# Kernel optimization log

Hardware: AMD Instinct MI355X
Metric: run time of the kernel (lower is better)

Reference implementation:

```python
import jax, jax.numpy as jnp
import numpy as np
from jax import lax

B, N, IN, OUT, RANK, P = 8, 7057, 1024, 1024, 64, 84
ALPHA = 1
SCALING = ALPHA / RANK
RATES = (2, 1, 4)


def _cubic(t):
    # PyTorch bicubic kernel (a = -0.75)
    a = -0.75
    at = jnp.abs(t)
    w1 = ((a + 2.0) * at - (a + 3.0)) * at * at + 1.0
    w2 = (((at - 5.0) * at + 8.0) * at - 4.0) * a
    return jnp.where(at <= 1.0, w1, jnp.where(at < 2.0, w2, 0.0))


def _resize_axis(x, out_size, axis):
    # 1-D bicubic resize along `axis`, align_corners=False, border replicate
    in_size = x.shape[axis]
    scale = in_size / out_size
    src = (jnp.arange(out_size, dtype=jnp.float32) + 0.5) * scale - 0.5
    i0 = jnp.floor(src)
    offs = jnp.arange(-1, 3, dtype=jnp.float32)[:, None]  # [4,1]
    pos = i0[None, :] + offs                              # [4,out]
    w = _cubic(src[None, :] - pos)                        # [4,out]
    idx = jnp.clip(pos.astype(jnp.int32), 0, in_size - 1)
    g = jnp.take(x, idx, axis=axis)  # axis -> (4, out)
    wshape = [1] * g.ndim
    wshape[axis] = 4
    wshape[axis + 1] = out_size
    return jnp.sum(g * w.reshape(wshape), axis=axis)


def _bicubic(x, h, w):
    # x: [B,C,H,W] -> [B,C,h,w]
    x = _resize_axis(x, h, axis=2)
    return _resize_axis(x, w, axis=3)


def _expert(x, cw, cb, rate):
    # x: [B,C,H,W]; cw: [C,C,3,3]; cb: [C]
    b, c, h, w = x.shape
    y = _bicubic(x, h * rate, w * rate)
    y = lax.conv_general_dilated(y, cw, (1, 1), [(1, 1), (1, 1)],
                                 dimension_numbers=('NCHW', 'OIHW', 'NCHW'))
    y = y + cb[None, :, None, None]
    y = _bicubic(y, h, w)
    return y.transpose(0, 2, 3, 1).reshape(b, h * w, c)  # [B,HW,C]


def setup_inputs() -> dict:
    key = jax.random.key(0)
    ks = jax.random.split(key, 9)
    return {
        'x': jax.random.normal(ks[0], (B, N, IN), dtype=jnp.float32),
        'W0': jax.random.normal(ks[1], (OUT, IN), dtype=jnp.float32) * 0.02,
        'b0': jax.random.normal(ks[2], (OUT,), dtype=jnp.float32) * 0.02,
        'W_down': jax.random.normal(ks[3], (RANK, IN), dtype=jnp.float32) * 0.02,
        'W_gate': jax.random.uniform(ks[4], (3, RANK), dtype=jnp.float32),
        'b_gate': jax.random.normal(ks[5], (3,), dtype=jnp.float32) * 0.02,
        'conv_w': jax.random.normal(ks[6], (3, RANK, RANK, 3, 3), dtype=jnp.float32) * 0.05,
        'conv_b': jax.random.normal(ks[7], (3, RANK), dtype=jnp.float32) * 0.02,
        'W_up': jax.random.normal(ks[8], (OUT, RANK), dtype=jnp.float32) * 0.02,
    }


def reference(x, W0, b0, W_down, W_gate, b_gate, conv_w, conv_b, W_up):
    out = jnp.einsum('bni,oi->bno', x, W0) + b0            # original layer
    z = jnp.einsum('bni,ri->bnr', x, W_down)               # lora_down (dropout p=0)
    cls_embed = z[:, :1]                                    # [B,1,R]
    feat = z[:, 1:].reshape(B, P, P, RANK).transpose(0, 3, 1, 2)  # [B,R,P,P]
    pooled = feat.mean(axis=(2, 3))                         # AdaptiveAvgPool2d(1)
    gate_score = pooled @ W_gate.T + b_gate                 # [B,3]
    gate_idx = jnp.argmax(gate_score, axis=-1)              # [B]
    eouts = jnp.stack([_expert(feat, conv_w[i], conv_b[i], RATES[i])
                       for i in range(3)], axis=0)          # [3,B,HW,R]
    sel = eouts[gate_idx, jnp.arange(B)] * SCALING          # [B,HW,R]
    lora = jnp.concatenate([cls_embed, sel], axis=1)        # [B,N,R]
    lora_out = jnp.einsum('bnr,or->bno', lora, W_up)
    return out + lora_out
```

## Files before the change

### kernel.cpp

```cpp
#include <hip/hip_runtime.h>
#include <stdint.h>

typedef unsigned short u16;
typedef __bf16 bf16x8 __attribute__((ext_vector_type(8)));
typedef float f32x4 __attribute__((ext_vector_type(4)));

#define B_ 8
#define N_ 7057
#define MTOT 56456
#define SCALING_F (1.0f/64.0f)

#define Z_OFF    0ull
#define LORA_OFF 14452736ull
#define GIDX_OFF 21679104ull
#define CWT_OFF  21679360ull
#define W0B_OFF  21900544ull
#define WDB_OFF  23997696ull
#define WUB_OFF  24128768ull
#define UP_OFF   24259840ull
#define CO_OFF   139865344ull
#define XB_OFF   255470848ull
#define WS_FAST  371092736ull
#define UPB_STRIDE ((size_t)112896 * 64)

__device__ __forceinline__ u16 f2b(float f) {
  __bf16 h = (__bf16)f;
  union { __bf16 h; u16 u; } v; v.h = h; return v.u;
}
__device__ __forceinline__ float b2f(u16 u) {
  union { uint32_t i; float f; } v; v.i = ((uint32_t)u) << 16; return v.f;
}
__device__ __forceinline__ void gload_lds16(const void* g, void* l) {
  __builtin_amdgcn_global_load_lds(
      (const __attribute__((address_space(1))) uint32_t*)g,
      (__attribute__((address_space(3))) uint32_t*)l, 16, 0, 0);
}
__device__ __forceinline__ f32x4 mfma16(bf16x8 a, bf16x8 b, f32x4 c) {
  return __builtin_amdgcn_mfma_f32_16x16x32_bf16(a, b, c, 0, 0, 0);
}
__device__ __forceinline__ bf16x8 cvt8(float4 a, float4 b) {
  bf16x8 v;
  v[0] = (__bf16)a.x; v[1] = (__bf16)a.y; v[2] = (__bf16)a.z; v[3] = (__bf16)a.w;
  v[4] = (__bf16)b.x; v[5] = (__bf16)b.y; v[6] = (__bf16)b.z; v[7] = (__bf16)b.w;
  return v;
}
__device__ __forceinline__ float cubicw(float t) {
  const float a = -0.75f;
  float at = fabsf(t);
  float w1 = ((a + 2.0f) * at - (a + 3.0f)) * at * at + 1.0f;
  float w2 = (((at - 5.0f) * at + 8.0f) * at - 4.0f) * a;
  return at <= 1.0f ? w1 : (at < 2.0f ? w2 : 0.0f);
}
__device__ __forceinline__ int iclamp(int v, int lo, int hi) { return v < lo ? lo : (v > hi ? hi : v); }
__device__ __forceinline__ int rate_of(int e) { return e == 0 ? 2 : (e == 1 ? 1 : 4); }

__global__ __launch_bounds__(256) void cvtall_kernel(const float* __restrict__ W0, const float* __restrict__ Wd,
                                                     const float* __restrict__ Wup, u16* __restrict__ dst) {
  int i = (blockIdx.x * 256 + threadIdx.x) * 4;
  if (i >= 1179648) return;
  const float* src;
  if (i < 1048576)      src = W0 + i;
  else if (i < 1114112) src = Wd + (i - 1048576);
  else                  src = Wup + (i - 1114112);
  float4 v = *(const float4*)src;
  union { u16 u[4]; uint2 q; } p;
  p.u[0] = f2b(v.x); p.u[1] = f2b(v.y); p.u[2] = f2b(v.z); p.u[3] = f2b(v.w);
  *(uint2*)(dst + i) = p.q;
}

__global__ __launch_bounds__(256) void cvtx_kernel(const float* __restrict__ x, u16* __restrict__ xb) {
  size_t stride = (size_t)gridDim.x * 256 * 8;
  for (size_t i = ((size_t)blockIdx.x * 256 + threadIdx.x) * 8; i < (size_t)MTOT * 1024; i += stride) {
    float4 a = *(const float4*)(x + i);
    float4 b = *(const float4*)(x + i + 4);
    *(bf16x8*)(xb + i) = cvt8(a, b);
  }
}

__global__ __launch_bounds__(256) void zgemm_kernel(const float* __restrict__ x,
                                                    const u16* __restrict__ Wdb,
                                                    float* __restrict__ z,
                                                    u16* __restrict__ xb) {
  __shared__ u16 As[64 * 32];
  __shared__ u16 Bs[64 * 32];
  const int tid = threadIdx.x;
  const int lane = tid & 63;
  const int w = tid >> 6;
  const int row0 = blockIdx.x * 64;
  f32x4 acc[4] = {{0,0,0,0},{0,0,0,0},{0,0,0,0},{0,0,0,0}};
  const int srow = tid >> 2, sk8 = tid & 3;
  int arow = row0 + srow; if (arow >= MTOT) arow = MTOT - 1;
  const float* agf = x + (size_t)arow * 1024 + sk8 * 8;
  const u16* bg = Wdb + (size_t)srow * 1024 + sk8 * 8;
  u16* xbp = xb ? (xb + (size_t)arow * 1024 + sk8 * 8) : nullptr;
  u16* al = As + tid * 8;
  u16* bl = Bs + tid * 8;
  const int klo = (lane >> 4) * 8;
  for (int k0 = 0; k0 < 1024; k0 += 32) {
    gload_lds16(bg + k0, bl);
    float4 q0 = *(const float4*)(agf + k0);
    float4 q1 = *(const float4*)(agf + k0 + 4);
    bf16x8 cv = cvt8(q0, q1);
    *(bf16x8*)al = cv;
    if (xbp) *(bf16x8*)(xbp + k0) = cv;
    __syncthreads();
    bf16x8 a = *(const bf16x8*)(As + (w * 16 + (lane & 15)) * 32 + klo);
#pragma unroll
    for (int fc = 0; fc < 4; ++fc) {
      bf16x8 bb = *(const bf16x8*)(Bs + (fc * 16 + (lane & 15)) * 32 + klo);
      acc[fc] = mfma16(a, bb, acc[fc]);
    }
    __syncthreads();
  }
  const int crow = (lane >> 4) * 4, ccol = lane & 15;
#pragma unroll
  for (int fc = 0; fc < 4; ++fc) {
#pragma unroll
    for (int i = 0; i < 4; ++i) {
      int gr = row0 + w * 16 + crow + i;
      if (gr < MTOT) z[(size_t)gr * 64 + fc * 16 + ccol] = acc[fc][i];
    }
  }
}

__global__ __launch_bounds__(256) void convwt_kernel(const float* __restrict__ cw, u16* __restrict__ cwt) {
  int idx = blockIdx.x * 256 + threadIdx.x;
  if (idx >= 3 * 9 * 64 * 64) return;
  int ci = idx & 63;
  int co = (idx >> 6) & 63;
  int rest = idx >> 12;
  int tap = rest % 9;
  int e = rest / 9;
  int sw = ((((ci >> 3) ^ (co & 7)) << 3) | (ci & 7));
  cwt[(((size_t)rest * 64) + co) * 64 + sw] = f2b(cw[((size_t)(e * 64 + co) * 64 + ci) * 9 + tap]);
}

__global__ __launch_bounds__(256) void gate1_kernel(const float* __restrict__ z, float* __restrict__ pp) {
  int b = blockIdx.y, q = blockIdx.x;
  int tid = threadIdx.x;
  int c = tid & 63, part = tid >> 6;
  const float* zb = z + (size_t)b * N_ * 64;
  int n0 = 1 + q * 126;
  float s = 0.0f;
  for (int n = n0 + part; n < n0 + 126; n += 4) s += zb[(size_t)n * 64 + c];
  __shared__ float red[4][64];
  red[part][c] = s;
  __syncthreads();
  if (tid < 64)
    pp[((size_t)b * 56 + q) * 64 + tid] = red[0][tid] + red[1][tid] + red[2][tid] + red[3][tid];
}

__global__ __launch_bounds__(64) void gate2_kernel(const float* __restrict__ pp, const float* __restrict__ z,
                                                   const float* __restrict__ Wg, const float* __restrict__ bg,
                                                   int* __restrict__ gidx, u16* __restrict__ lora) {
  int b = blockIdx.x;
  int c = threadIdx.x;
  float s = 0.0f;
  for (int q = 0; q < 56; ++q) s += pp[((size_t)b * 56 + q) * 64 + c];
  __shared__ float pl[64];
  pl[c] = s * (1.0f / 7056.0f);
  const float* zb = z + (size_t)b * N_ * 64;
  lora[(size_t)b * N_ * 64 + c] = f2b(zb[c]);
  __syncthreads();
  if (c == 0) {
    float best = 0.0f; int bi = 0;
    for (int e = 0; e < 3; ++e) {
      float sc = bg[e];
      for (int r = 0; r < 64; ++r) sc += pl[r] * Wg[e * 64 + r];
      if (e == 0 || sc > best) { best = sc; bi = e; }
    }
    gidx[b] = bi;
  }
}

__global__ __launch_bounds__(256) void conv_kernel(const float* __restrict__ z, const u16* __restrict__ cwt,
                                                   const float* __restrict__ cb, const int* __restrict__ gidx,
                                                   u16* __restrict__ cvo) {
  int b = blockIdx.z;
  int e = gidx[b];
  int r = rate_of(e);
  int H = 84 * r;
  int tx = blockIdx.x, ty = blockIdx.y;
  if (tx * 8 >= H || ty * 8 >= H) return;
  __shared__ u16 halo[100 * 64];
  __shared__ u16 Bw[2][4096];
  __shared__ float hw[100][8];
  __shared__ int hidx[100][8];
  int tid = threadIdx.x, lane = tid & 63, w = tid >> 6;
  const float* zb = z + ((size_t)b * N_ + 1) * 64;
  const u16* wte = cwt + (size_t)e * 9 * 4096;
  gload_lds16(wte + tid * 8, Bw[0] + tid * 8);
  gload_lds16(wte + 2048 + tid * 8, Bw[0] + 2048 + tid * 8);
  float inv = 1.0f / (float)r;
  if (tid < 100) {
    int hy = tid / 10, hx = tid - hy * 10;
    int iy = ty * 8 - 1 + hy, ix = tx * 8 - 1 + hx;
    float sy = (iy + 0.5f) * inv - 0.5f;
    float fy = floorf(sy);
    int iy0 = (int)fy;
    float sx = (ix + 0.5f) * inv - 0.5f;
    float fx = floorf(sx);
    int ix0 = (int)fx;
#pragma unroll
    for (int u = 0; u < 4; ++u) {
      hw[tid][u] = cubicw(sy - (fy - 1.0f + u));
      hidx[tid][u] = iclamp(iy0 - 1 + u, 0, 83) * (84 * 64);
      hw[tid][4 + u] = cubicw(sx - (fx - 1.0f + u));
      hidx[tid][4 + u] = iclamp(ix0 - 1 + u, 0, 83) * 64;
    }
  }
  __syncthreads();
  for (int li = tid; li < 800; li += 256) {
    int pix = li >> 3, cq = li & 7;
    int hy = pix / 10, hx = pix - hy * 10;
    int iy = ty * 8 - 1 + hy, ix = tx * 8 - 1 + hx;
    bf16x8 o;
#pragma unroll
    for (int t = 0; t < 8; ++t) o[t] = (__bf16)0.0f;
    if (iy >= 0 && iy < H && ix >= 0 && ix < H) {
      float a8[8] = {0.f,0.f,0.f,0.f,0.f,0.f,0.f,0.f};
#pragma unroll
      for (int u = 0; u < 4; ++u) {
        const float* zr = zb + hidx[pix][u] + cq * 8;
        float wyu = hw[pix][u];
#pragma unroll
        for (int v = 0; v < 4; ++v) {
          float wuv = wyu * hw[pix][4 + v];
          const float* zp = zr + hidx[pix][4 + v];
          float4 q0 = *(const float4*)zp;
          float4 q1 = *(const float4*)(zp + 4);
          a8[0] += wuv * q0.x; a8[1] += wuv * q0.y; a8[2] += wuv * q0.z; a8[3] += wuv * q0.w;
          a8[4] += wuv * q1.x; a8[5] += wuv * q1.y; a8[6] += wuv * q1.z; a8[7] += wuv * q1.w;
        }
      }
#pragma unroll
      for (int t = 0; t < 8; ++t) o[t] = (__bf16)a8[t];
    }
    *(bf16x8*)(halo + pix * 64 + (((cq ^ (pix & 7)) << 3))) = o;
  }
  __syncthreads();
  f32x4 acc[4] = {{0,0,0,0},{0,0,0,0},{0,0,0,0},{0,0,0,0}};
  int p = w * 16 + (lane & 15);
  int py = p >> 3, px = p & 7;
  int kg = lane >> 4;
  for (int tap = 0; tap < 9; ++tap) {
    if (tap < 8) {
      const u16* wt = wte + (size_t)(tap + 1) * 4096;
      gload_lds16(wt + tid * 8, Bw[(tap + 1) & 1] + tid * 8);
      gload_lds16(wt + 2048 + tid * 8, Bw[(tap + 1) & 1] + 2048 + tid * 8);
    }
    int dy = tap / 3, dx = tap - dy * 3;
    int pr = (py + dy) * 10 + (px + dx);
    const u16* bwc = Bw[tap & 1];
#pragma unroll
    for (int kk = 0; kk < 2; ++kk) {
      int ch = kk * 4 + kg;
      bf16x8 a = *(const bf16x8*)(halo + pr * 64 + (((ch ^ (pr & 7)) << 3)));
#pragma unroll
      for (int fc = 0; fc < 4; ++fc) {
        int co = fc * 16 + (lane & 15);
        bf16x8 bb = *(const bf16x8*)(bwc + co * 64 + (((ch ^ (co & 7)) << 3)));
        acc[fc] = mfma16(a, bb, acc[fc]);
      }
    }
    __syncthreads();
  }
  int crow = (lane >> 4) * 4, ccol = lane & 15;
  u16* cvb = cvo + (size_t)b * UPB_STRIDE;
#pragma unroll
  for (int fc = 0; fc < 4; ++fc) {
    int co = fc * 16 + ccol;
    float bias = cb[e * 64 + co];
#pragma unroll
    for (int i = 0; i < 4; ++i) {
      int pd = w * 16 + crow + i;
      int gy = ty * 8 + (pd >> 3), gx = tx * 8 + (pd & 7);
      if (gy < H && gx < H)
        cvb[((size_t)gy * H + gx) * 64 + co] = f2b(acc[fc][i] + bias);
    }
  }
}

__global__ __launch_bounds__(256) void down_kernel(const u16* __restrict__ cvo, const int* __restrict__ gidx,
                                                   u16* __restrict__ lora) {
  int b = blockIdx.z;
  int r = rate_of(gidx[b]);
  int H = 84 * r;
  int tid = threadIdx.x;
  int c = tid & 63, s = tid >> 6;
  int y = blockIdx.y;
  int x = blockIdx.x * 4 + s;
  float fr = (float)r;
  float sy = (y + 0.5f) * fr - 0.5f;
  float fy = floorf(sy);
  int iy0 = (int)fy;
  float wy[4]; int yi[4];
#pragma unroll
  for (int u = 0; u < 4; ++u) { wy[u] = cubicw(sy - (fy - 1.0f + u)); yi[u] = iclamp(iy0 - 1 + u, 0, H - 1); }
  float sx = (x + 0.5f) * fr - 0.5f;
  float fx = floorf(sx);
  int ix0 = (int)fx;
  float wx[4]; int xi[4];
#pragma unroll
  for (int v = 0; v < 4; ++v) { wx[v] = cubicw(sx - (fx - 1.0f + v)); xi[v] = iclamp(ix0 - 1 + v, 0, H - 1); }
  const u16* cbase = cvo + (size_t)b * UPB_STRIDE;
  float acc = 0.0f;
#pragma unroll
  for (int u = 0; u < 4; ++u)
#pragma unroll
    for (int v = 0; v < 4; ++v)
      acc += wy[u] * wx[v] * b2f(cbase[((size_t)yi[u] * H + xi[v]) * 64 + c]);
  lora[((size_t)b * N_ + 1 + y * 84 + x) * 64 + c] = f2b(acc * SCALING_F);
}

__global__ __launch_bounds__(256) void main_gemm(const u16* __restrict__ xb, const u16* __restrict__ W0b,
                                                 const float* __restrict__ b0, const u16* __restrict__ lora,
                                                 const u16* __restrict__ Wub, float* __restrict__ out) {
  __shared__ u16 As[128 * 64];
  __shared__ u16 Bs[128 * 64];
  int tid = threadIdx.x, lane = tid & 63, w = tid >> 6;
  int bid = blockIdx.x;
  int wg = (bid & 7) * 442 + (bid >> 3);
  int row0 = (wg >> 3) * 128, col0 = (wg & 7) * 128;
  int wr = w >> 1, wc = w & 1;
  f32x4 acc[4][4] = {};
  int srow = tid >> 3;
  int schunk = tid & 7;
  int sch8 = ((schunk ^ (srow & 7)) << 3);
  int ar[4]; int br[4];
  u16* aldst[4]; u16* bldst[4];
#pragma unroll
  for (int p = 0; p < 4; ++p) {
    int rr = row0 + p * 32 + srow;
    ar[p] = rr >= MTOT ? MTOT - 1 : rr;
    br[p] = col0 + p * 32 + srow;
    aldst[p] = As + (p * 32 + srow) * 64 + schunk * 8;
    bldst[p] = Bs + (p * 32 + srow) * 64 + schunk * 8;
  }
  for (int k0 = 0; k0 < 1024; k0 += 64) {
#pragma unroll
    for (int p = 0; p < 4; ++p)
      gload_lds16(xb + (size_t)ar[p] * 1024 + k0 + sch8, aldst[p]);
#pragma unroll
    for (int p = 0; p < 4; ++p)
      gload_lds16(W0b + (size_t)br[p] * 1024 + k0 + sch8, bldst[p]);
    __syncthreads();
#pragma unroll
    for (int kk = 0; kk < 2; ++kk) {
      int pc = (((kk << 2) + (lane >> 4)) ^ (lane & 7)) << 3;
      bf16x8 af[4], bfr[4];
#pragma unroll
      for (int fm = 0; fm < 4; ++fm)
        af[fm] = *(const bf16x8*)(As + (wr * 64 + fm * 16 + (lane & 15)) * 64 + pc);
#pragma unroll
      for (int fc = 0; fc < 4; ++fc)
        bfr[fc] = *(const bf16x8*)(Bs + (wc * 64 + fc * 16 + (lane & 15)) * 64 + pc);
#pragma unroll
      for (int fm = 0; fm < 4; ++fm)
#pragma unroll
        for (int fc = 0; fc < 4; ++fc)
          acc[fm][fc] = mfma16(af[fm], bfr[fc], acc[fm][fc]);
    }
    __syncthreads();
  }
#pragma unroll
  for (int p = 0; p < 4; ++p)
    gload_lds16(lora + (size_t)ar[p] * 64 + sch8, aldst[p]);
#pragma unroll
  for (int p = 0; p < 4; ++p)
    gload_lds16(Wub + (size_t)br[p] * 64 + sch8, bldst[p]);
  __syncthreads();
#pragma unroll
  for (int kk = 0; kk < 2; ++kk) {
    int pc = (((kk << 2) + (lane >> 4)) ^ (lane & 7)) << 3;
    bf16x8 af[4], bfr[4];
#pragma unroll
    for (int fm = 0; fm < 4; ++fm)
      af[fm] = *(const bf16x8*)(As + (wr * 64 + fm * 16 + (lane & 15)) * 64 + pc);
#pragma unroll
    for (int fc = 0; fc < 4; ++fc)
      bfr[fc] = *(const bf16x8*)(Bs + (wc * 64 + fc * 16 + (lane & 15)) * 64 + pc);
#pragma unroll
    for (int fm = 0; fm < 4; ++fm)
#pragma unroll
      for (int fc = 0; fc < 4; ++fc)
        acc[fm][fc] = mfma16(af[fm], bfr[fc], acc[fm][fc]);
  }
  __syncthreads();
  int crow = (lane >> 4) * 4, ccol = lane & 15;
#pragma unroll
  for (int fm = 0; fm < 4; ++fm) {
    int grb = row0 + wr * 64 + fm * 16 + crow;
#pragma unroll
    for (int fc = 0; fc < 4; ++fc) {
      int gc = col0 + wc * 64 + fc * 16 + ccol;
      float bias = b0[gc];
#pragma unroll
      for (int i = 0; i < 4; ++i) {
        int gr = grb + i;
        if (gr < MTOT) out[(size_t)gr * 1024 + gc] = acc[fm][fc][i] + bias;
      }
    }
  }
}

extern "C" void kernel_launch(void* const* d_in, const int* in_sizes, int n_in,
                              void* d_out, int out_size, void* d_ws, size_t ws_size,
                              hipStream_t stream) {
  const float* x   = (const float*)d_in[0];
  const float* W0  = (const float*)d_in[1];
  const float* b0  = (const float*)d_in[2];
  const float* Wd  = (const float*)d_in[3];
  const float* Wg  = (const float*)d_in[4];
  const float* bg  = (const float*)d_in[5];
  const float* cw  = (const float*)d_in[6];
  const float* cb  = (const float*)d_in[7];
  const float* Wup = (const float*)d_in[8];
  char* ws = (char*)d_ws;
  float* z    = (float*)(ws + Z_OFF);
  u16* lora   = (u16*)(ws + LORA_OFF);
  int* gidx   = (int*)(ws + GIDX_OFF);
  u16* cwt    = (u16*)(ws + CWT_OFF);
  u16* W0b    = (u16*)(ws + W0B_OFF);
  u16* Wdb    = (u16*)(ws + WDB_OFF);
  u16* Wub    = (u16*)(ws + WUB_OFF);
  float* pp   = (float*)(ws + UP_OFF);
  u16* cvo    = (u16*)(ws + CO_OFF);
  float* out  = (float*)d_out;

  const bool fast = ws_size >= WS_FAST;
  u16* xb = fast ? (u16*)(ws + XB_OFF) : (u16*)(ws + CO_OFF);

  cvtall_kernel<<<dim3(1152), dim3(256), 0, stream>>>(W0, Wd, Wup, W0b);
  convwt_kernel<<<dim3(432), dim3(256), 0, stream>>>(cw, cwt);
  zgemm_kernel<<<dim3(883), dim3(256), 0, stream>>>(x, Wdb, z, fast ? xb : nullptr);
  gate1_kernel<<<dim3(56, 8), dim3(256), 0, stream>>>(z, pp);
  gate2_kernel<<<dim3(8), dim3(64), 0, stream>>>(pp, z, Wg, bg, gidx, lora);
  conv_kernel<<<dim3(42, 42, 8), dim3(256), 0, stream>>>(z, cwt, cb, gidx, cvo);
  down_kernel<<<dim3(21, 84, 8), dim3(256), 0, stream>>>(cvo, gidx, lora);
  if (!fast)
    cvtx_kernel<<<dim3(2048), dim3(256), 0, stream>>>(x, xb);
  main_gemm<<<dim3(3536), dim3(256), 0, stream>>>(xb, W0b, b0, lora, Wub, out);
}
```

Baseline: 546.9 us.

## Stage low-res z patch in LDS for upsample halo and skip interpolation at rate 1

For upsample rates 2 and 4, the conv kernel now async-loads a small clamped patch of the low-resolution z feature map into shared memory. It then runs the 4x4 bicubic gather from LDS instead of issuing 16 scattered global loads per halo pixel. For rate 1 the bicubic weights are identity, so the halo is filled by a direct load and bf16 conversion. This adds 16 KB of LDS per block, which may reduce occupancy, and it relies on the patch sizes (8 and 6) covering every tap.

```diff
diff --git a/kernel.cpp b/kernel.cpp
--- a/kernel.cpp
+++ b/kernel.cpp
@@ -182,6 +182,7 @@
   int H = 84 * r;
   int tx = blockIdx.x, ty = blockIdx.y;
   if (tx * 8 >= H || ty * 8 >= H) return;
+  __shared__ __align__(16) float patch[8 * 8 * 64];
   __shared__ u16 halo[100 * 64];
   __shared__ u16 Bw[2][4096];
   __shared__ float hw[100][8];
@@ -191,54 +192,82 @@
   const u16* wte = cwt + (size_t)e * 9 * 4096;
   gload_lds16(wte + tid * 8, Bw[0] + tid * 8);
   gload_lds16(wte + 2048 + tid * 8, Bw[0] + 2048 + tid * 8);
-  float inv = 1.0f / (float)r;
-  if (tid < 100) {
-    int hy = tid / 10, hx = tid - hy * 10;
-    int iy = ty * 8 - 1 + hy, ix = tx * 8 - 1 + hx;
-    float sy = (iy + 0.5f) * inv - 0.5f;
-    float fy = floorf(sy);
-    int iy0 = (int)fy;
-    float sx = (ix + 0.5f) * inv - 0.5f;
-    float fx = floorf(sx);
-    int ix0 = (int)fx;
-#pragma unroll
-    for (int u = 0; u < 4; ++u) {
-      hw[tid][u] = cubicw(sy - (fy - 1.0f + u));
-      hidx[tid][u] = iclamp(iy0 - 1 + u, 0, 83) * (84 * 64);
-      hw[tid][4 + u] = cubicw(sx - (fx - 1.0f + u));
-      hidx[tid][4 + u] = iclamp(ix0 - 1 + u, 0, 83) * 64;
-    }
-  }
-  __syncthreads();
-  for (int li = tid; li < 800; li += 256) {
-    int pix = li >> 3, cq = li & 7;
-    int hy = pix / 10, hx = pix - hy * 10;
-    int iy = ty * 8 - 1 + hy, ix = tx * 8 - 1 + hx;
-    bf16x8 o;
-#pragma unroll
-    for (int t = 0; t < 8; ++t) o[t] = (__bf16)0.0f;
-    if (iy >= 0 && iy < H && ix >= 0 && ix < H) {
-      float a8[8] = {0.f,0.f,0.f,0.f,0.f,0.f,0.f,0.f};
+  if (r == 1) {
+    for (int li = tid; li < 800; li += 256) {
+      int pix = li >> 3, cq = li & 7;
+      int hy = pix / 10, hx = pix - hy * 10;
+      int iy = ty * 8 - 1 + hy, ix = tx * 8 - 1 + hx;
+      bf16x8 o;
+#pragma unroll
+      for (int t = 0; t < 8; ++t) o[t] = (__bf16)0.0f;
+      if (iy >= 0 && iy < 84 && ix >= 0 && ix < 84) {
+        const float* zp = zb + ((size_t)iy * 84 + ix) * 64 + cq * 8;
+        float4 q0 = *(const float4*)zp;
+        float4 q1 = *(const float4*)(zp + 4);
+        o = cvt8(q0, q1);
+      }
+      *(bf16x8*)(halo + pix * 64 + ((cq ^ (pix & 7)) << 3)) = o;
+    }
+    __syncthreads();
+  } else {
+    const int P = (r == 2) ? 8 : 6;
+    float inv = 1.0f / (float)r;
+    int by = (int)floorf((ty * 8 - 0.5f) * inv - 0.5f) - 1;
+    int bx = (int)floorf((tx * 8 - 0.5f) * inv - 0.5f) - 1;
+    for (int li = tid; li < P * P * 16; li += 256) {
+      int pp_ = li >> 4, f4 = li & 15;
+      int py = pp_ / P, px = pp_ - py * P;
+      int zr = iclamp(by + py, 0, 83), zc = iclamp(bx + px, 0, 83);
+      gload_lds16(zb + ((size_t)zr * 84 + zc) * 64 + f4 * 4, patch + (size_t)li * 4);
+    }
+    if (tid < 100) {
+      int hy = tid / 10, hx = tid - hy * 10;
+      int iy = ty * 8 - 1 + hy, ix = tx * 8 - 1 + hx;
+      float sy = (iy + 0.5f) * inv - 0.5f;
+      float fy = floorf(sy);
+      int iy0 = (int)fy;
+      float sx = (ix + 0.5f) * inv - 0.5f;
+      float fx = floorf(sx);
+      int ix0 = (int)fx;
 #pragma unroll
       for (int u = 0; u < 4; ++u) {
-        const float* zr = zb + hidx[pix][u] + cq * 8;
-        float wyu = hw[pix][u];
-#pragma unroll
-        for (int v = 0; v < 4; ++v) {
-          float wuv = wyu * hw[pix][4 + v];
-          const float* zp = zr + hidx[pix][4 + v];
-          float4 q0 = *(const float4*)zp;
-          float4 q1 = *(const float4*)(zp + 4);
-          a8[0] += wuv * q0.x; a8[1] += wuv * q0.y; a8[2] += wuv * q0.z; a8[3] += wuv * q0.w;
-          a8[4] += wuv * q1.x; a8[5] += wuv * q1.y; a8[6] += wuv * q1.z; a8[7] += wuv * q1.w;
+        hw[tid][u] = cubicw(sy - (fy - 1.0f + u));
+        hidx[tid][u] = (iclamp(iy0 - 1 + u, 0, 83) - by) * (P * 64);
+        hw[tid][4 + u] = cubicw(sx - (fx - 1.0f + u));
+        hidx[tid][4 + u] = (iclamp(ix0 - 1 + u, 0, 83) - bx) * 64;
+      }
+    }
+    __syncthreads();
+    for (int li = tid; li < 800; li += 256) {
+      int pix = li >> 3, cq = li & 7;
+      int hy = pix / 10, hx = pix - hy * 10;
+      int iy = ty * 8 - 1 + hy, ix = tx * 8 - 1 + hx;
+      bf16x8 o;
+#pragma unroll
+      for (int t = 0; t < 8; ++t) o[t] = (__bf16)0.0f;
+      if (iy >= 0 && iy < H && ix >= 0 && ix < H) {
+        float a8[8] = {0.f,0.f,0.f,0.f,0.f,0.f,0.f,0.f};
+#pragma unroll
+        for (int u = 0; u < 4; ++u) {
+          const float* prow = patch + hidx[pix][u] + cq * 8;
+          float wyu = hw[pix][u];
+#pragma unroll
+          for (int v = 0; v < 4; ++v) {
+            float wuv = wyu * hw[pix][4 + v];
+            const float* pz = prow + hidx[pix][4 + v];
+            float4 q0 = *(const float4*)pz;
+            float4 q1 = *(const float4*)(pz + 4);
+            a8[0] += wuv * q0.x; a8[1] += wuv * q0.y; a8[2] += wuv * q0.z; a8[3] += wuv * q0.w;
+            a8[4] += wuv * q1.x; a8[5] += wuv * q1.y; a8[6] += wuv * q1.z; a8[7] += wuv * q1.w;
+          }
         }
+#pragma unroll
+        for (int t = 0; t < 8; ++t) o[t] = (__bf16)a8[t];
       }
-#pragma unroll
-      for (int t = 0; t < 8; ++t) o[t] = (__bf16)a8[t];
-    }
-    *(bf16x8*)(halo + pix * 64 + (((cq ^ (pix & 7)) << 3))) = o;
-  }
-  __syncthreads();
+      *(bf16x8*)(halo + pix * 64 + ((cq ^ (pix & 7)) << 3)) = o;
+    }
+    __syncthreads();
+  }
   f32x4 acc[4] = {{0,0,0,0},{0,0,0,0},{0,0,0,0},{0,0,0,0}};
   int p = w * 16 + (lane & 15);
   int py = p >> 3, px = p & 7;
@@ -255,11 +284,11 @@
 #pragma unroll
     for (int kk = 0; kk < 2; ++kk) {
       int ch = kk * 4 + kg;
-      bf16x8 a = *(const bf16x8*)(halo + pr * 64 + (((ch ^ (pr & 7)) << 3)));
+      bf16x8 a = *(const bf16x8*)(halo + pr * 64 + ((ch ^ (pr & 7)) << 3));
 #pragma unroll
       for (int fc = 0; fc < 4; ++fc) {
         int co = fc * 16 + (lane & 15);
-        bf16x8 bb = *(const bf16x8*)(bwc + co * 64 + (((ch ^ (co & 7)) << 3)));
+        bf16x8 bb = *(const bf16x8*)(bwc + co * 64 + ((ch ^ (co & 7)) << 3));
         acc[fc] = mfma16(a, bb, acc[fc]);
       }
     }
```

New measurement: 520.2 us (median of 4 runs). -4.9%, faster.
